# Optimization experiments

Hardware: AMD Instinct MI355X
Metric: run time of the kernel (lower is better)

The kernel has to match this reference:

```python
import jax, jax.numpy as jnp
import numpy as np

N, C, SI, VI, H, R = 10000, 2, 128, 16, 4, 32
SH, VH = SI // H, VI // H  # 32, 4
EPS = 1e-8

def _vnorm(x, axis):
    # clamped L2 norm, matches _norm_no_nan
    return jnp.sqrt(jnp.clip(jnp.sum(x * x, axis=axis), EPS, None))

def _gvp_full(s, v, wh, ws_w, ws_b, wv, wsv_w, wsv_b):
    # GVP with activations=(silu, sigmoid), vector_gate=True, vi=vo
    vh = jnp.swapaxes(v, -1, -2) @ wh            # [..., 3, h]
    vn = _vnorm(vh, -2)                          # [..., h]
    so = jnp.concatenate([s, vn], -1) @ ws_w + ws_b
    vo = jnp.swapaxes(vh @ wv, -1, -2)           # [..., vo, 3]
    gate = jax.nn.sigmoid(jax.nn.sigmoid(so) @ wsv_w + wsv_b)
    return jax.nn.silu(so), vo * gate[..., None]

def setup_inputs():
    key = jax.random.key(0)
    ks = iter(jax.random.split(key, 40))
    def lin(i, o):
        return jax.random.normal(next(ks), (i, o), jnp.float32) / np.sqrt(i)
    def bias(o):
        return 0.02 * jax.random.normal(next(ks), (o,), jnp.float32)
    inp = {}
    inp['s'] = jax.random.normal(next(ks), (N, C, SI), jnp.float32)
    inp['v'] = jax.random.normal(next(ks), (N, C, VI, 3), jnp.float32)
    # weight_proj: GVP((SI,VI)->(R,0)), no activations; h_dim = max(VI,0) = VI
    inp['wp_wh'] = lin(VI, VI); inp['wp_ws_w'] = lin(VI + SI, R); inp['wp_ws_b'] = bias(R)
    # to_q/k/v: GVP((SI,VI)->(SI,VI)), silu/sigmoid, vector_gate; h_dim = VI
    for p in ('q', 'k', 'vv'):
        inp[p + '_wh'] = lin(VI, VI)
        inp[p + '_ws_w'] = lin(VI + SI, SI); inp[p + '_ws_b'] = bias(SI)
        inp[p + '_wv'] = lin(VI, VI)
        inp[p + '_wsv_w'] = lin(SI, VI); inp[p + '_wsv_b'] = bias(VI)
    # attn_gvp_long: GVP((2*SH, 2*VH) -> (1,0)), no activations; h_dim = 2*VH
    inp['attn_wh'] = lin(2 * VH, 2 * VH)
    inp['attn_ws_w'] = lin(2 * VH + 2 * SH, 1); inp['attn_ws_b'] = bias(1)
    return inp

def reference(s, v, wp_wh, wp_ws_w, wp_ws_b,
              q_wh, q_ws_w, q_ws_b, q_wv, q_wsv_w, q_wsv_b,
              k_wh, k_ws_w, k_ws_b, k_wv, k_wsv_w, k_wsv_b,
              vv_wh, vv_ws_w, vv_ws_b, vv_wv, vv_wsv_w, vv_wsv_b,
              attn_wh, attn_ws_w, attn_ws_b):
    n, c = s.shape[:2]
    # ---- Compress: softmax-pool N -> R anchors ----
    vh = jnp.swapaxes(v, -1, -2) @ wp_wh          # [N,C,3,VI]
    vn = _vnorm(vh, -2)                            # [N,C,VI]
    pw = jnp.concatenate([s, vn], -1) @ wp_ws_w + wp_ws_b  # [N,C,R]
    pw = jax.nn.softmax(pw, axis=0)                # softmax over nodes
    s_g = jnp.einsum('nca,ncs->acs', pw, s)        # [R,C,SI] (includes transpose(0,1))
    v_g = jnp.einsum('nca,ncvd->acvd', pw, v)      # [R,C,VI,3]
    # ---- q from nodes, k/v from anchors ----
    qs, qv = _gvp_full(s, v, q_wh, q_ws_w, q_ws_b, q_wv, q_wsv_w, q_wsv_b)
    ks, kv = _gvp_full(s_g, v_g, k_wh, k_ws_w, k_ws_b, k_wv, k_wsv_w, k_wsv_b)
    vs, vv_ = _gvp_full(s_g, v_g, vv_wh, vv_ws_w, vv_ws_b, vv_wv, vv_wsv_w, vv_wsv_b)
    qs = qs.reshape(n, c, H, SH); qv = qv.reshape(n, c, H, VH, 3)
    ks = ks.reshape(R, c, H, SH); kv = kv.reshape(R, c, H, VH, 3)
    vs = vs.reshape(R, c, H, SH); vv_ = vv_.reshape(R, c, H, VH, 3)
    # ---- attention GVP on cat(q, k): split weights instead of materializing concat ----
    wh_q, wh_k = attn_wh[:VH], attn_wh[VH:]        # wh @ cat(qv,kv) = qv@wh_q + kv@wh_k
    qh = jnp.swapaxes(qv, -1, -2) @ wh_q           # [N,C,H,3,2VH]
    kh = jnp.swapaxes(kv, -1, -2) @ wh_k           # [R,C,H,3,2VH]
    vn2 = _vnorm(qh[:, None] + kh[None], -2)       # [N,R,C,H,2VH]
    ws_q = attn_ws_w[:SH]; ws_k = attn_ws_w[SH:2 * SH]; ws_n = attn_ws_w[2 * SH:]
    e = (qs @ ws_q)[:, None] + (ks @ ws_k)[None] + vn2 @ ws_n + attn_ws_b  # [N,R,C,H,1]
    e = e[..., 0] / np.sqrt(SH)
    alpha = jax.nn.softmax(e, axis=1)              # softmax over anchors (dim=1)
    # ---- Broadcast: weighted sum of anchor values ----
    out_s = jnp.einsum('nrch,rchd->nchd', alpha, vs).reshape(n, c, SI)
    out_v = jnp.einsum('nrch,rchde->nchde', alpha, vv_).reshape(n, c, VI, 3)
    return out_s, out_v
```

## Files before the change

kernel.cpp:

```cpp
#include <hip/hip_runtime.h>
#include <hip/hip_bf16.h>


#define N_  10000
#define C_  2
#define SI_ 128
#define VI_ 16
#define H_  4
#define R_  32
#define SH_ 32
#define VH_ 4
#define NC_ (N_*C_)

#define ROWS_ 16
#define XSTR_ 20

typedef const float* __restrict__ fptr;

__device__ __forceinline__ float sigm(float x){ return 1.f/(1.f+__expf(-x)); }

#define OFF_LG   0
#define OFF_EQH  640000
#define OFF_SG   2640000
#define OFF_TKH  2651520
#define OFF_TEK  2657664
#define OFF_TVS  2657920
#define OFF_TVV  2666112

#define SGSTRIDE_ 180

__global__ __launch_bounds__(256) void kA(
    fptr s, fptr v,
    fptr wp_wh, fptr wp_ws_w, fptr wp_ws_b,
    fptr q_wh, fptr q_ws_w, fptr q_ws_b, fptr q_wv, fptr q_wsv_w, fptr q_wsv_b,
    fptr attn_wh, fptr attn_ws_w,
    float* __restrict__ pexp, float* __restrict__ eqh,
    float* __restrict__ sgz)
{
  __shared__ __align__(16) float ARENA[160*XSTR_];
  __shared__ __align__(16) float VVs[ROWS_*48];
  __shared__ __align__(16) float VHQ[ROWS_*48];
  __shared__ __align__(16) float SO[ROWS_*128];
  __shared__ __align__(16) float GATE[ROWS_*16];
  __shared__ __align__(16) float QV[ROWS_*48];
  float* const XT  = ARENA;
  float* const SIG = ARENA;

  const int tid  = threadIdx.x;
  const int row0 = blockIdx.x * ROWS_;

  if (blockIdx.x == 0){
    for (int i = tid; i < 64*SGSTRIDE_; i += 256) sgz[i] = 0.f;
  }

  for (int idx = tid; idx < ROWS_*128; idx += 256){
    int r = idx >> 7, j = idx & 127;
    XT[j*XSTR_ + r] = s[(row0+r)*128 + j];
  }
  for (int idx = tid; idx < ROWS_*48; idx += 256){
    int r = idx / 48, k = idx - r*48;
    VVs[r*48 + k] = v[(row0+r)*48 + k];
  }
  __syncthreads();

  for (int idx = tid; idx < ROWS_*32; idx += 256){
    int r = idx >> 5, ii = idx & 31, path = ii >> 4, i = ii & 15;
    fptr wh = path ? wp_wh : q_wh;
    float h0=0.f, h1=0.f, h2=0.f;
    #pragma unroll
    for (int j = 0; j < 16; j++){
      float w = wh[j*16 + i];
      h0 = fmaf(VVs[r*48 + j*3 + 0], w, h0);
      h1 = fmaf(VVs[r*48 + j*3 + 1], w, h1);
      h2 = fmaf(VVs[r*48 + j*3 + 2], w, h2);
    }
    float vn = sqrtf(fmaxf(h0*h0 + h1*h1 + h2*h2, 1e-8f));
    if (!path){
      VHQ[r*48 +  0 + i] = h0;
      VHQ[r*48 + 16 + i] = h1;
      VHQ[r*48 + 32 + i] = h2;
      XT[(128+i)*XSTR_ + r] = vn;
    } else {
      XT[(144+i)*XSTR_ + r] = vn;
    }
  }
  __syncthreads();

  const int colA = tid & 127, rgA = tid >> 7;
  float acc[8];
  {
    float bqs = q_ws_b[colA];
    #pragma unroll
    for (int k = 0; k < 8; k++) acc[k] = bqs;
    const float* xbA = &XT[rgA*8];
    #pragma unroll 8
    for (int j = 0; j < 144; j++){
      float w = q_ws_w[j*128 + colA];
      const float* xb = xbA + j*XSTR_;
      float4 x0 = *(const float4*)(xb + 0);
      float4 x1 = *(const float4*)(xb + 4);
      acc[0] = fmaf(x0.x, w, acc[0]); acc[1] = fmaf(x0.y, w, acc[1]);
      acc[2] = fmaf(x0.z, w, acc[2]); acc[3] = fmaf(x0.w, w, acc[3]);
      acc[4] = fmaf(x1.x, w, acc[4]); acc[5] = fmaf(x1.y, w, acc[5]);
      acc[6] = fmaf(x1.z, w, acc[6]); acc[7] = fmaf(x1.w, w, acc[7]);
    }
  }
  {
    const int colB = tid & 31, rgB = tid >> 5;
    float b0 = wp_ws_b[colB];
    float a0 = b0, a1 = b0;
    #pragma unroll 8
    for (int j = 0; j < 144; j++){
      int jj = (j < 128) ? j : (j + 16);
      float w = wp_ws_w[j*32 + colB];
      const float* xb = &XT[jj*XSTR_ + rgB*2];
      a0 = fmaf(xb[0], w, a0);
      a1 = fmaf(xb[1], w, a1);
    }
    const int n = (row0 >> 1) + rgB;
    pexp[(0*32 + colB)*N_ + n] = __expf(a0);
    pexp[(1*32 + colB)*N_ + n] = __expf(a1);
  }
  __syncthreads();

  #pragma unroll
  for (int k = 0; k < 8; k++){
    float so = acc[k];
    float sg_ = sigm(so);
    SIG[(rgA*8 + k)*128 + colA] = sg_;
    SO [(rgA*8 + k)*128 + colA] = so * sg_;
  }
  __syncthreads();

  {
    const int r = tid >> 4, g = tid & 15;
    float ga = q_wsv_b[g];
    #pragma unroll 8
    for (int o = 0; o < 128; o += 4){
      float4 s4 = *(const float4*)&SIG[r*128 + o];
      ga = fmaf(s4.x, q_wsv_w[(o+0)*16 + g], ga);
      ga = fmaf(s4.y, q_wsv_w[(o+1)*16 + g], ga);
      ga = fmaf(s4.z, q_wsv_w[(o+2)*16 + g], ga);
      ga = fmaf(s4.w, q_wsv_w[(o+3)*16 + g], ga);
    }
    GATE[r*16 + g] = sigm(ga);
  }
  __syncthreads();

  for (int t = tid; t < 64 + ROWS_*48; t += 256){
    if (t < 64){
      const int r = t >> 2, h = t & 3;
      float e = 0.f;
      #pragma unroll
      for (int u = 0; u < 32; u++)
        e = fmaf(SO[r*128 + h*32 + u], attn_ws_w[u], e);
      eqh[(row0 + r)*100 + h] = e;
    } else {
      const int t2 = t - 64;
      int r = t2 / 48, k = t2 - r*48, i = k / 3, d = k - i*3;
      float a = 0.f;
      #pragma unroll
      for (int j = 0; j < 16; j++)
        a = fmaf(VHQ[r*48 + d*16 + j], q_wv[j*16 + i], a);
      QV[r*48 + k] = a * GATE[r*16 + i];
    }
  }
  __syncthreads();

  for (int t = tid; t < ROWS_*96; t += 256){
    int r = t / 96, k = t - r*96;
    int h = k / 24, rem = k - h*24, d = rem >> 3, ee = rem & 7;
    float a = 0.f;
    #pragma unroll
    for (int i = 0; i < 4; i++)
      a = fmaf(QV[r*48 + (h*4 + i)*3 + d], attn_wh[i*8 + ee], a);
    eqh[(row0 + r)*100 + 8 + k] = a;
  }
}

__global__ __launch_bounds__(256) void kAccum(const float* __restrict__ pexp,
                                              fptr s, fptr v,
                                              float* __restrict__ sg)
{
  const int b = blockIdx.x;
  const int c = b & 1, ah = (b >> 1) & 1, chunk = b >> 2;
  const int n0 = chunk * 50;
  const int tid = threadIdx.x;
  const int ag = tid >> 6, dl = tid & 63;
  const int abase = ah*16 + ag*4;

  const float* pb = pexp + (c*32 + abase)*N_;
  float acc[4][3] = {};
  float dn[4] = {};

  #pragma unroll 2
  for (int n = n0; n < n0 + 50; n++){
    const int rc = n*2 + c;
    float pw[4];
    #pragma unroll
    for (int aa = 0; aa < 4; aa++){
      pw[aa] = pb[aa*N_ + n];
      dn[aa] += pw[aa];
    }
    #pragma unroll
    for (int dd = 0; dd < 3; dd++){
      int d = dl + 64*dd;
      if (d < 176){
        float xv = (d < 128) ? s[rc*128 + d] : v[rc*48 + d - 128];
        #pragma unroll
        for (int aa = 0; aa < 4; aa++)
          acc[aa][dd] = fmaf(pw[aa], xv, acc[aa][dd]);
      }
    }
  }
  #pragma unroll
  for (int aa = 0; aa < 4; aa++){
    const int base = (c*32 + abase + aa)*SGSTRIDE_;
    #pragma unroll
    for (int dd = 0; dd < 3; dd++){
      int d = dl + 64*dd;
      if (d < 176) atomicAdd(&sg[base + d], acc[aa][dd]);
    }
    if (dl == 0) atomicAdd(&sg[base + 176], dn[aa]);
  }
}

__global__ __launch_bounds__(256) void kSmall(
    const float* __restrict__ sg,
    fptr k_wh, fptr k_ws_w, fptr k_ws_b, fptr k_wv, fptr k_wsv_w, fptr k_wsv_b,
    fptr vv_wh, fptr vv_ws_w, fptr vv_ws_b, fptr vv_wv, fptr vv_wsv_w, fptr vv_wsv_b,
    fptr attn_wh, fptr attn_ws_w,
    float* __restrict__ tkh, float* __restrict__ tek,
    float* __restrict__ tvs, float* __restrict__ tvv)
{
  const int b = blockIdx.x, r = b >> 1, c = b & 1;
  const int tid = threadIdx.x;
  __shared__ float X[176];
  __shared__ float VN[2][16];
  __shared__ float VH[2][48];
  __shared__ float SOk[128], SOv[128];
  __shared__ float G[2][16];
  __shared__ float KV[48];

  if (tid < 176){
    const float* p = sg + (c*32 + r)*SGSTRIDE_;
    X[tid] = p[tid] / p[176];
  }
  __syncthreads();

  if (tid < 32){
    int path = tid >> 4, i = tid & 15;
    fptr wh = path ? vv_wh : k_wh;
    float h0=0.f, h1=0.f, h2=0.f;
    #pragma unroll
    for (int j = 0; j < 16; j++){
      float w = wh[j*16 + i];
      h0 = fmaf(X[128 + j*3 + 0], w, h0);
      h1 = fmaf(X[128 + j*3 + 1], w, h1);
      h2 = fmaf(X[128 + j*3 + 2], w, h2);
    }
    VH[path][ 0 + i] = h0; VH[path][16 + i] = h1; VH[path][32 + i] = h2;
    VN[path][i] = sqrtf(fmaxf(h0*h0 + h1*h1 + h2*h2, 1e-8f));
  }
  __syncthreads();

  {
    int path = tid >> 7, col = tid & 127;
    fptr W  = path ? vv_ws_w : k_ws_w;
    fptr Bb = path ? vv_ws_b : k_ws_b;
    float so = Bb[col];
    for (int j = 0; j < 128; j++) so = fmaf(X[j], W[j*128 + col], so);
    #pragma unroll
    for (int i = 0; i < 16; i++)  so = fmaf(VN[path][i], W[(128+i)*128 + col], so);
    (path ? SOv : SOk)[col] = so;
  }
  __syncthreads();

  if (tid < 32){
    int path = tid >> 4, g = tid & 15;
    fptr Wsv = path ? vv_wsv_w : k_wsv_w;
    fptr Bsv = path ? vv_wsv_b : k_wsv_b;
    const float* SOp = path ? SOv : SOk;
    float ga = Bsv[g];
    for (int o = 0; o < 128; o++)
      ga = fmaf(sigm(SOp[o]), Wsv[o*16 + g], ga);
    G[path][g] = sigm(ga);
  } else if (tid < 36){
    int h = tid - 32;
    float e = 0.f;
    #pragma unroll
    for (int t = 0; t < 32; t++){
      float so = SOk[h*32 + t];
      e = fmaf(so * sigm(so), attn_ws_w[32 + t], e);
    }
    tek[(r*2 + c)*4 + h] = e;
  } else if (tid >= 64 && tid < 192){
    int o = tid - 64;
    float so = SOv[o];
    tvs[(r*2 + c)*128 + o] = so * sigm(so);
  }
  __syncthreads();

  if (tid < 96){
    int path = tid / 48, k = tid % 48, i = k / 3, d = k - i*3;
    fptr Wv = path ? vv_wv : k_wv;
    float vo = 0.f;
    #pragma unroll
    for (int j = 0; j < 16; j++)
      vo = fmaf(VH[path][d*16 + j], Wv[j*16 + i], vo);
    float gv = vo * G[path][i];
    if (path == 0) KV[k] = gv;
    else {
      int h = i >> 2, ii = i & 3;
      tvv[(((r*2 + c)*4 + h)*4 + ii)*3 + d] = gv;
    }
  }
  __syncthreads();

  if (tid < 96){
    int h = tid / 24, rem = tid % 24, d = rem >> 3, ee = rem & 7;
    float a = 0.f;
    #pragma unroll
    for (int i = 0; i < 4; i++)
      a = fmaf(KV[(h*4 + i)*3 + d], attn_wh[(4 + i)*8 + ee], a);
    tkh[((r*2 + c)*4 + h)*24 + d*8 + ee] = a;
  }
}

__global__ __launch_bounds__(512, 1) void kAttn(
    const float* __restrict__ eqh,
    const float* __restrict__ tkh, const float* __restrict__ tek,
    const float* __restrict__ tvs, const float* __restrict__ tvv,
    fptr attn_ws_w, fptr attn_ws_b,
    float* __restrict__ out)
{
  __shared__ __align__(16) float KH[6144];
  __shared__ __align__(16) float EK[256];
  __shared__ __align__(16) float VS[256*36];
  __shared__ __align__(16) float VVt[3072];
  const int tid = threadIdx.x;

  for (int i = tid; i < 6144; i += 512) KH[i] = tkh[i];
  if (tid < 256) EK[tid] = tek[tid];
  for (int i = tid; i < 8192; i += 512){ int base = i >> 5, t = i & 31; VS[base*36 + t] = tvs[i]; }
  for (int i = tid; i < 3072; i += 512) VVt[i] = tvv[i];

  float wsn[8];
  #pragma unroll
  for (int ee = 0; ee < 8; ee++) wsn[ee] = attn_ws_w[64 + ee];
  const float wb = attn_ws_b[0];
  __syncthreads();

  const int row = blockIdx.x*128 + (tid >> 2);
  const int h = tid & 3;
  if (row < NC_){
    const int c = row & 1;
    const float eq = eqh[row*100 + h];
    float qh[24];
    {
      const float4* qp = (const float4*)&eqh[row*100 + 8 + h*24];
      #pragma unroll
      for (int k = 0; k < 6; k++){
        float4 t4 = qp[k];
        qh[k*4+0] = t4.x; qh[k*4+1] = t4.y; qh[k*4+2] = t4.z; qh[k*4+3] = t4.w;
      }
    }
    float4 accs4[8];
    float4 accv4[3];
    #pragma unroll
    for (int q = 0; q < 8; q++) accs4[q] = make_float4(0.f,0.f,0.f,0.f);
    #pragma unroll
    for (int q = 0; q < 3; q++) accv4[q] = make_float4(0.f,0.f,0.f,0.f);
    float den = 0.f;

    #pragma unroll
    for (int r = 0; r < 32; r++){
      const int base = (r*2 + c)*4 + h;
      const float* khp = &KH[base*24];
      float en = 0.f;
      #pragma unroll
      for (int ee = 0; ee < 8; ee++){
        float a0 = qh[ee]      + khp[ee];
        float a1 = qh[8 + ee]  + khp[8 + ee];
        float a2 = qh[16 + ee] + khp[16 + ee];
        en = fmaf(sqrtf(fmaxf(a0*a0 + a1*a1 + a2*a2, 1e-8f)), wsn[ee], en);
      }
      const float w = __expf((eq + EK[base] + en + wb) * 0.17677669529663687f);
      den += w;
      const float4* vp4 = (const float4*)&VS[base*36];
      #pragma unroll
      for (int q = 0; q < 8; q++){
        float4 t4 = vp4[q];
        accs4[q].x = fmaf(w, t4.x, accs4[q].x);
        accs4[q].y = fmaf(w, t4.y, accs4[q].y);
        accs4[q].z = fmaf(w, t4.z, accs4[q].z);
        accs4[q].w = fmaf(w, t4.w, accs4[q].w);
      }
      const float4* vv4 = (const float4*)&VVt[base*12];
      #pragma unroll
      for (int q = 0; q < 3; q++){
        float4 t4 = vv4[q];
        accv4[q].x = fmaf(w, t4.x, accv4[q].x);
        accv4[q].y = fmaf(w, t4.y, accv4[q].y);
        accv4[q].z = fmaf(w, t4.z, accv4[q].z);
        accv4[q].w = fmaf(w, t4.w, accv4[q].w);
      }
    }
    const float inv = 1.f / den;
    float4* po = (float4*)&out[row*128 + h*32];
    #pragma unroll
    for (int q = 0; q < 8; q++){
      float4 t4 = accs4[q];
      t4.x *= inv; t4.y *= inv; t4.z *= inv; t4.w *= inv;
      po[q] = t4;
    }
    float4* pv = (float4*)&out[NC_*128 + row*48 + h*12];
    #pragma unroll
    for (int q = 0; q < 3; q++){
      float4 t4 = accv4[q];
      t4.x *= inv; t4.y *= inv; t4.z *= inv; t4.w *= inv;
      pv[q] = t4;
    }
  }
}

extern "C" void kernel_launch(void* const* d_in, const int* in_sizes, int n_in,
                              void* d_out, int out_size, void* d_ws, size_t ws_size,
                              hipStream_t stream)
{
  fptr s        = (fptr)d_in[0];
  fptr v        = (fptr)d_in[1];
  fptr wp_wh    = (fptr)d_in[2];
  fptr wp_ws_w  = (fptr)d_in[3];
  fptr wp_ws_b  = (fptr)d_in[4];
  fptr q_wh     = (fptr)d_in[5];
  fptr q_ws_w   = (fptr)d_in[6];
  fptr q_ws_b   = (fptr)d_in[7];
  fptr q_wv     = (fptr)d_in[8];
  fptr q_wsv_w  = (fptr)d_in[9];
  fptr q_wsv_b  = (fptr)d_in[10];
  fptr k_wh     = (fptr)d_in[11];
  fptr k_ws_w   = (fptr)d_in[12];
  fptr k_ws_b   = (fptr)d_in[13];
  fptr k_wv     = (fptr)d_in[14];
  fptr k_wsv_w  = (fptr)d_in[15];
  fptr k_wsv_b  = (fptr)d_in[16];
  fptr vv_wh    = (fptr)d_in[17];
  fptr vv_ws_w  = (fptr)d_in[18];
  fptr vv_ws_b  = (fptr)d_in[19];
  fptr vv_wv    = (fptr)d_in[20];
  fptr vv_wsv_w = (fptr)d_in[21];
  fptr vv_wsv_b = (fptr)d_in[22];
  fptr attn_wh  = (fptr)d_in[23];
  fptr attn_ws_w= (fptr)d_in[24];
  fptr attn_ws_b= (fptr)d_in[25];

  float* ws   = (float*)d_ws;
  float* pexp = ws + OFF_LG;
  float* eqh  = ws + OFF_EQH;
  float* sg   = ws + OFF_SG;
  float* tkh  = ws + OFF_TKH;
  float* tek  = ws + OFF_TEK;
  float* tvs  = ws + OFF_TVS;
  float* tvv  = ws + OFF_TVV;

  kA<<<NC_/ROWS_, 256, 0, stream>>>(s, v, wp_wh, wp_ws_w, wp_ws_b,
                                    q_wh, q_ws_w, q_ws_b, q_wv, q_wsv_w, q_wsv_b,
                                    attn_wh, attn_ws_w, pexp, eqh, sg);
  kAccum<<<800, 256, 0, stream>>>(pexp, s, v, sg);
  kSmall<<<64, 256, 0, stream>>>(sg,
                                 k_wh, k_ws_w, k_ws_b, k_wv, k_wsv_w, k_wsv_b,
                                 vv_wh, vv_ws_w, vv_ws_b, vv_wv, vv_wsv_w, vv_wsv_b,
                                 attn_wh, attn_ws_w, tkh, tek, tvs, tvv);
  kAttn<<<(NC_ + 127)/128, 512, 0, stream>>>(eqh, tkh, tek, tvs, tvv,
                                             attn_ws_w, attn_ws_b, (float*)d_out);
}
```

Baseline: 241.7 us.

## Read s directly from global in kA projections and reduce eq via wave shuffles

The transposed shared-memory staging of s in kernel kA is removed. Both the q-scalar projection and the weight_proj projection now read s rows straight from global memory as wave-uniform float4 loads, and the vector-norm features are kept in a small separate shared buffer. The per-head attention dot product is now computed from the accumulator registers with xor-shuffle reductions, which drops the SO buffer and one barrier. The cost is redundant global/L1 reads of s across waves in exchange for less shared-memory traffic and LDS footprint.

```diff
diff --git a/kernel.cpp b/kernel.cpp
--- a/kernel.cpp
+++ b/kernel.cpp
@@ -13,7 +13,6 @@
 #define NC_ (N_*C_)
 
 #define ROWS_ 16
-#define XSTR_ 20
 
 typedef const float* __restrict__ fptr;
 
@@ -37,26 +36,22 @@
     float* __restrict__ pexp, float* __restrict__ eqh,
     float* __restrict__ sgz)
 {
-  __shared__ __align__(16) float ARENA[160*XSTR_];
+  __shared__ __align__(16) float SIG[ROWS_*128];
+  __shared__ __align__(16) float VN[2][16*16];
   __shared__ __align__(16) float VVs[ROWS_*48];
   __shared__ __align__(16) float VHQ[ROWS_*48];
-  __shared__ __align__(16) float SO[ROWS_*128];
   __shared__ __align__(16) float GATE[ROWS_*16];
   __shared__ __align__(16) float QV[ROWS_*48];
-  float* const XT  = ARENA;
-  float* const SIG = ARENA;
 
   const int tid  = threadIdx.x;
+  const int lane = tid & 63;
+  const int wv   = __builtin_amdgcn_readfirstlane(tid >> 6);
   const int row0 = blockIdx.x * ROWS_;
 
   if (blockIdx.x == 0){
     for (int i = tid; i < 64*SGSTRIDE_; i += 256) sgz[i] = 0.f;
   }
 
-  for (int idx = tid; idx < ROWS_*128; idx += 256){
-    int r = idx >> 7, j = idx & 127;
-    XT[j*XSTR_ + r] = s[(row0+r)*128 + j];
-  }
   for (int idx = tid; idx < ROWS_*48; idx += 256){
     int r = idx / 48, k = idx - r*48;
     VVs[r*48 + k] = v[(row0+r)*48 + k];
@@ -79,56 +74,111 @@
       VHQ[r*48 +  0 + i] = h0;
       VHQ[r*48 + 16 + i] = h1;
       VHQ[r*48 + 32 + i] = h2;
-      XT[(128+i)*XSTR_ + r] = vn;
+      VN[0][i*16 + r] = vn;
     } else {
-      XT[(144+i)*XSTR_ + r] = vn;
-    }
-  }
-  __syncthreads();
-
-  const int colA = tid & 127, rgA = tid >> 7;
+      VN[1][i*16 + r] = vn;
+    }
+  }
+  __syncthreads();
+
+  const int col = (wv & 1)*64 + lane;
+  const int rw0 = (wv >> 1)*8;
+  const float* __restrict__ srow = s + (size_t)(row0 + rw0)*128;
   float acc[8];
   {
-    float bqs = q_ws_b[colA];
+    float bqs = q_ws_b[col];
     #pragma unroll
     for (int k = 0; k < 8; k++) acc[k] = bqs;
-    const float* xbA = &XT[rgA*8];
-    #pragma unroll 8
-    for (int j = 0; j < 144; j++){
-      float w = q_ws_w[j*128 + colA];
-      const float* xb = xbA + j*XSTR_;
-      float4 x0 = *(const float4*)(xb + 0);
-      float4 x1 = *(const float4*)(xb + 4);
-      acc[0] = fmaf(x0.x, w, acc[0]); acc[1] = fmaf(x0.y, w, acc[1]);
-      acc[2] = fmaf(x0.z, w, acc[2]); acc[3] = fmaf(x0.w, w, acc[3]);
-      acc[4] = fmaf(x1.x, w, acc[4]); acc[5] = fmaf(x1.y, w, acc[5]);
-      acc[6] = fmaf(x1.z, w, acc[6]); acc[7] = fmaf(x1.w, w, acc[7]);
-    }
-  }
+    #pragma unroll 2
+    for (int jb = 0; jb < 128; jb += 4){
+      float w0 = q_ws_w[(jb+0)*128 + col];
+      float w1 = q_ws_w[(jb+1)*128 + col];
+      float w2 = q_ws_w[(jb+2)*128 + col];
+      float w3 = q_ws_w[(jb+3)*128 + col];
+      #pragma unroll
+      for (int k = 0; k < 8; k++){
+        float4 x = *(const float4*)(srow + k*128 + jb);
+        acc[k] = fmaf(x.x, w0, acc[k]);
+        acc[k] = fmaf(x.y, w1, acc[k]);
+        acc[k] = fmaf(x.z, w2, acc[k]);
+        acc[k] = fmaf(x.w, w3, acc[k]);
+      }
+    }
+    #pragma unroll
+    for (int i = 0; i < 16; i++){
+      float w = q_ws_w[(128+i)*128 + col];
+      float4 xa = *(const float4*)&VN[0][i*16 + rw0];
+      float4 xb = *(const float4*)&VN[0][i*16 + rw0 + 4];
+      acc[0] = fmaf(xa.x, w, acc[0]); acc[1] = fmaf(xa.y, w, acc[1]);
+      acc[2] = fmaf(xa.z, w, acc[2]); acc[3] = fmaf(xa.w, w, acc[3]);
+      acc[4] = fmaf(xb.x, w, acc[4]); acc[5] = fmaf(xb.y, w, acc[5]);
+      acc[6] = fmaf(xb.z, w, acc[6]); acc[7] = fmaf(xb.w, w, acc[7]);
+    }
+  }
+
   {
-    const int colB = tid & 31, rgB = tid >> 5;
-    float b0 = wp_ws_b[colB];
-    float a0 = b0, a1 = b0;
-    #pragma unroll 8
-    for (int j = 0; j < 144; j++){
-      int jj = (j < 128) ? j : (j + 16);
-      float w = wp_ws_w[j*32 + colB];
-      const float* xb = &XT[jj*XSTR_ + rgB*2];
-      a0 = fmaf(xb[0], w, a0);
-      a1 = fmaf(xb[1], w, a1);
-    }
-    const int n = (row0 >> 1) + rgB;
-    pexp[(0*32 + colB)*N_ + n] = __expf(a0);
-    pexp[(1*32 + colB)*N_ + n] = __expf(a1);
-  }
-  __syncthreads();
-
-  #pragma unroll
-  for (int k = 0; k < 8; k++){
-    float so = acc[k];
-    float sg_ = sigm(so);
-    SIG[(rgA*8 + k)*128 + colA] = sg_;
-    SO [(rgA*8 + k)*128 + colA] = so * sg_;
+    const int colB = lane & 31;
+    const int rw0b = wv*4;
+    const float* __restrict__ srb = s + (size_t)(row0 + rw0b)*128;
+    float bb = wp_ws_b[colB];
+    float b4[4];
+    #pragma unroll
+    for (int k = 0; k < 4; k++) b4[k] = bb;
+    #pragma unroll 2
+    for (int jb = 0; jb < 128; jb += 4){
+      float w0 = wp_ws_w[(jb+0)*32 + colB];
+      float w1 = wp_ws_w[(jb+1)*32 + colB];
+      float w2 = wp_ws_w[(jb+2)*32 + colB];
+      float w3 = wp_ws_w[(jb+3)*32 + colB];
+      #pragma unroll
+      for (int k = 0; k < 4; k++){
+        float4 x = *(const float4*)(srb + k*128 + jb);
+        b4[k] = fmaf(x.x, w0, b4[k]);
+        b4[k] = fmaf(x.y, w1, b4[k]);
+        b4[k] = fmaf(x.z, w2, b4[k]);
+        b4[k] = fmaf(x.w, w3, b4[k]);
+      }
+    }
+    #pragma unroll
+    for (int i = 0; i < 16; i++){
+      float w = wp_ws_w[(128+i)*32 + colB];
+      float4 xv = *(const float4*)&VN[1][i*16 + rw0b];
+      b4[0] = fmaf(xv.x, w, b4[0]);
+      b4[1] = fmaf(xv.y, w, b4[1]);
+      b4[2] = fmaf(xv.z, w, b4[2]);
+      b4[3] = fmaf(xv.w, w, b4[3]);
+    }
+    if (lane < 32){
+      #pragma unroll
+      for (int k = 0; k < 4; k++){
+        const int gr = row0 + rw0b + k;
+        pexp[((gr & 1)*32 + colB)*N_ + (gr >> 1)] = __expf(b4[k]);
+      }
+    }
+  }
+
+  {
+    const float weq = attn_ws_w[col & 31];
+    float e[8];
+    #pragma unroll
+    for (int k = 0; k < 8; k++){
+      float so  = acc[k];
+      float sg_ = sigm(so);
+      SIG[(rw0 + k)*128 + col] = sg_;
+      e[k] = so * sg_ * weq;
+    }
+    #pragma unroll
+    for (int m = 1; m <= 16; m <<= 1){
+      #pragma unroll
+      for (int k = 0; k < 8; k++)
+        e[k] += __shfl_xor(e[k], m, 64);
+    }
+    if ((lane & 31) == 0){
+      const int h = col >> 5;
+      #pragma unroll
+      for (int k = 0; k < 8; k++)
+        eqh[(row0 + rw0 + k)*100 + h] = e[k];
+    }
   }
   __syncthreads();
 
@@ -147,23 +197,13 @@
   }
   __syncthreads();
 
-  for (int t = tid; t < 64 + ROWS_*48; t += 256){
-    if (t < 64){
-      const int r = t >> 2, h = t & 3;
-      float e = 0.f;
-      #pragma unroll
-      for (int u = 0; u < 32; u++)
-        e = fmaf(SO[r*128 + h*32 + u], attn_ws_w[u], e);
-      eqh[(row0 + r)*100 + h] = e;
-    } else {
-      const int t2 = t - 64;
-      int r = t2 / 48, k = t2 - r*48, i = k / 3, d = k - i*3;
-      float a = 0.f;
-      #pragma unroll
-      for (int j = 0; j < 16; j++)
-        a = fmaf(VHQ[r*48 + d*16 + j], q_wv[j*16 + i], a);
-      QV[r*48 + k] = a * GATE[r*16 + i];
-    }
+  for (int t = tid; t < ROWS_*48; t += 256){
+    int r = t / 48, k = t - r*48, i = k / 3, d = k - i*3;
+    float a = 0.f;
+    #pragma unroll
+    for (int j = 0; j < 16; j++)
+      a = fmaf(VHQ[r*48 + d*16 + j], q_wv[j*16 + i], a);
+    QV[r*48 + k] = a * GATE[r*16 + i];
   }
   __syncthreads();
 
```

New measurement: 278.0 us. 1.15x slower.

## Split attention kernel by head and anchor range, reduce via wavefront shuffles

Applied to the files above, without the earlier changes.

The attention kernel now launches one block per (row tile, head), so each block stages only that head's anchor keys and values in shared memory, with padded strides. Within a block, four lanes split the 32 anchors of one row and head, and their partial softmax numerators and denominators are combined with xor shuffles before one lane writes. The aim is more blocks, lower shared-memory use per block and shorter serial loops, giving higher occupancy and latency hiding. In exchange, each row's query data is loaded four times and the shuffle reductions add work. The un-normalised exponent has no max subtraction, as before.

```diff
diff --git a/kernel.cpp b/kernel.cpp
--- a/kernel.cpp
+++ b/kernel.cpp
@@ -327,23 +327,34 @@
   }
 }
 
-__global__ __launch_bounds__(512, 1) void kAttn(
+__global__ __launch_bounds__(256) void kAttn(
     const float* __restrict__ eqh,
     const float* __restrict__ tkh, const float* __restrict__ tek,
     const float* __restrict__ tvs, const float* __restrict__ tvv,
     fptr attn_ws_w, fptr attn_ws_b,
     float* __restrict__ out)
 {
-  __shared__ __align__(16) float KH[6144];
-  __shared__ __align__(16) float EK[256];
-  __shared__ __align__(16) float VS[256*36];
-  __shared__ __align__(16) float VVt[3072];
+  __shared__ __align__(16) float KH[64*28];
+  __shared__ __align__(16) float VS[64*36];
+  __shared__ __align__(16) float VV[64*12];
+  __shared__ float EK[64];
   const int tid = threadIdx.x;
-
-  for (int i = tid; i < 6144; i += 512) KH[i] = tkh[i];
-  if (tid < 256) EK[tid] = tek[tid];
-  for (int i = tid; i < 8192; i += 512){ int base = i >> 5, t = i & 31; VS[base*36 + t] = tvs[i]; }
-  for (int i = tid; i < 3072; i += 512) VVt[i] = tvv[i];
+  const int h      = blockIdx.x & 3;
+  const int rowblk = blockIdx.x >> 2;
+
+  for (int i = tid; i < 64*24; i += 256){
+    int m = i / 24, t = i - m*24;
+    KH[m*28 + t] = tkh[(m*4 + h)*24 + t];
+  }
+  for (int i = tid; i < 64*32; i += 256){
+    int m = i >> 5, t = i & 31;
+    VS[m*36 + t] = tvs[m*128 + h*32 + t];
+  }
+  for (int i = tid; i < 64*12; i += 256){
+    int m = i / 12, t = i - m*12;
+    VV[m*12 + t] = tvv[(m*4 + h)*12 + t];
+  }
+  if (tid < 64) EK[tid] = tek[tid*4 + h];
 
   float wsn[8];
   #pragma unroll
@@ -351,8 +362,8 @@
   const float wb = attn_ws_b[0];
   __syncthreads();
 
-  const int row = blockIdx.x*128 + (tid >> 2);
-  const int h = tid & 3;
+  const int rh  = tid & 3;
+  const int row = rowblk*64 + (tid >> 2);
   if (row < NC_){
     const int c = row & 1;
     const float eq = eqh[row*100 + h];
@@ -374,9 +385,9 @@
     float den = 0.f;
 
     #pragma unroll
-    for (int r = 0; r < 32; r++){
-      const int base = (r*2 + c)*4 + h;
-      const float* khp = &KH[base*24];
+    for (int rr = 0; rr < 8; rr++){
+      const int m = (rh*8 + rr)*2 + c;
+      const float* khp = &KH[m*28];
       float en = 0.f;
       #pragma unroll
       for (int ee = 0; ee < 8; ee++){
@@ -385,9 +396,9 @@
         float a2 = qh[16 + ee] + khp[16 + ee];
         en = fmaf(sqrtf(fmaxf(a0*a0 + a1*a1 + a2*a2, 1e-8f)), wsn[ee], en);
       }
-      const float w = __expf((eq + EK[base] + en + wb) * 0.17677669529663687f);
+      const float w = __expf((eq + EK[m] + en + wb) * 0.17677669529663687f);
       den += w;
-      const float4* vp4 = (const float4*)&VS[base*36];
+      const float4* vp4 = (const float4*)&VS[m*36];
       #pragma unroll
       for (int q = 0; q < 8; q++){
         float4 t4 = vp4[q];
@@ -396,7 +407,7 @@
         accs4[q].z = fmaf(w, t4.z, accs4[q].z);
         accs4[q].w = fmaf(w, t4.w, accs4[q].w);
       }
-      const float4* vv4 = (const float4*)&VVt[base*12];
+      const float4* vv4 = (const float4*)&VV[m*12];
       #pragma unroll
       for (int q = 0; q < 3; q++){
         float4 t4 = vv4[q];
@@ -406,20 +417,48 @@
         accv4[q].w = fmaf(w, t4.w, accv4[q].w);
       }
     }
-    const float inv = 1.f / den;
-    float4* po = (float4*)&out[row*128 + h*32];
+
     #pragma unroll
     for (int q = 0; q < 8; q++){
-      float4 t4 = accs4[q];
-      t4.x *= inv; t4.y *= inv; t4.z *= inv; t4.w *= inv;
-      po[q] = t4;
-    }
-    float4* pv = (float4*)&out[NC_*128 + row*48 + h*12];
+      accs4[q].x += __shfl_xor(accs4[q].x, 1, 64);
+      accs4[q].x += __shfl_xor(accs4[q].x, 2, 64);
+      accs4[q].y += __shfl_xor(accs4[q].y, 1, 64);
+      accs4[q].y += __shfl_xor(accs4[q].y, 2, 64);
+      accs4[q].z += __shfl_xor(accs4[q].z, 1, 64);
+      accs4[q].z += __shfl_xor(accs4[q].z, 2, 64);
+      accs4[q].w += __shfl_xor(accs4[q].w, 1, 64);
+      accs4[q].w += __shfl_xor(accs4[q].w, 2, 64);
+    }
     #pragma unroll
     for (int q = 0; q < 3; q++){
-      float4 t4 = accv4[q];
-      t4.x *= inv; t4.y *= inv; t4.z *= inv; t4.w *= inv;
-      pv[q] = t4;
+      accv4[q].x += __shfl_xor(accv4[q].x, 1, 64);
+      accv4[q].x += __shfl_xor(accv4[q].x, 2, 64);
+      accv4[q].y += __shfl_xor(accv4[q].y, 1, 64);
+      accv4[q].y += __shfl_xor(accv4[q].y, 2, 64);
+      accv4[q].z += __shfl_xor(accv4[q].z, 1, 64);
+      accv4[q].z += __shfl_xor(accv4[q].z, 2, 64);
+      accv4[q].w += __shfl_xor(accv4[q].w, 1, 64);
+      accv4[q].w += __shfl_xor(accv4[q].w, 2, 64);
+    }
+    den += __shfl_xor(den, 1, 64);
+    den += __shfl_xor(den, 2, 64);
+
+    if (rh == 0){
+      const float inv = 1.f / den;
+      float4* po = (float4*)&out[row*128 + h*32];
+      #pragma unroll
+      for (int q = 0; q < 8; q++){
+        float4 t4 = accs4[q];
+        t4.x *= inv; t4.y *= inv; t4.z *= inv; t4.w *= inv;
+        po[q] = t4;
+      }
+      float4* pv = (float4*)&out[NC_*128 + row*48 + h*12];
+      #pragma unroll
+      for (int q = 0; q < 3; q++){
+        float4 t4 = accv4[q];
+        t4.x *= inv; t4.y *= inv; t4.z *= inv; t4.w *= inv;
+        pv[q] = t4;
+      }
     }
   }
 }
@@ -472,6 +511,6 @@
                                  k_wh, k_ws_w, k_ws_b, k_wv, k_wsv_w, k_wsv_b,
                                  vv_wh, vv_ws_w, vv_ws_b, vv_wv, vv_wsv_w, vv_wsv_b,
                                  attn_wh, attn_ws_w, tkh, tek, tvs, tvv);
-  kAttn<<<(NC_ + 127)/128, 512, 0, stream>>>(eqh, tkh, tek, tvs, tvv,
-                                             attn_ws_w, attn_ws_b, (float*)d_out);
+  kAttn<<<((NC_ + 63)/64)*4, 256, 0, stream>>>(eqh, tkh, tek, tvs, tvv,
+                                               attn_ws_w, attn_ws_b, (float*)d_out);
 }
```

New measurement: 232.8 us (median of 2 runs). -3.7%, faster.
